# Kernel tuning notes

Hardware: AMD Instinct MI355X
Metric: run time of the kernel (lower is better)

Reference implementation:

```python
import jax, jax.numpy as jnp
import numpy as np

EPS = 1e-12  # F.normalize default eps


def _l2norm(x, axis):
    n = jnp.sqrt(jnp.sum(x * x, axis=axis, keepdims=True))
    return x / jnp.maximum(n, EPS)


def setup_inputs() -> dict:
    key = jax.random.key(0)
    k1, k2, k3, k4 = jax.random.split(key, 4)
    N, T, C, K = 64, 577, 768, 64
    return {
        "grids": jax.random.normal(k1, (N, T, C), dtype=jnp.float32),
        "conv_w": jax.random.normal(k2, (K, C), dtype=jnp.float32) * 0.03,
        "conv_b": jax.random.normal(k3, (K,), dtype=jnp.float32) * 0.01,
        "centroids": jax.random.normal(k4, (K, C), dtype=jnp.float32) * 0.03,
    }


def reference(grids, conv_w, conv_b, centroids):
    # grids: (N, 577, 768) -> (N, C=768, T=577), matching view+permute in torch
    N = grids.shape[0]
    x = jnp.transpose(grids.reshape(N, 577, 768), (0, 2, 1))  # (N, C, T)
    # per-token L2 normalization over channel dim
    x = _l2norm(x, axis=1)
    # 1x1 conv == per-token linear: (N, K, T)
    logits = jnp.einsum('kc,nct->nkt', conv_w, x) + conv_b[None, :, None]
    a = jax.nn.softmax(logits, axis=1)  # softmax over regions K
    # NetVLAD algebraic rewrite of sum_t a[n,k,t]*(x[n,:,t]-c[k,:]):
    #   = (a @ x^T)[n,k,c] - sum_t(a)[n,k] * c[k,c]
    p = jnp.einsum('nkt,nct->nkc', a, x) - a.sum(axis=-1)[:, :, None] * centroids[None]
    p = _l2norm(p, axis=2)             # intra-region normalization
    p = p.reshape(N, -1)               # (N, K*C)
    p = _l2norm(p, axis=1)             # global normalization
    return p
```

## Files before the change

kernel.cpp:

```cpp
#include <hip/hip_runtime.h>
#include <hip/hip_bf16.h>
#include <math.h>

#define TT 577
#define TP 640
#define CCH 768
#define KR 64
#define NB 64
#define LSTR 136

typedef __attribute__((ext_vector_type(8))) short bf16x8;
typedef __attribute__((ext_vector_type(8))) unsigned short ushort8;
typedef __attribute__((ext_vector_type(4))) float f32x4;

static constexpr float EPSF = 1e-12f;

static __device__ inline unsigned short f2bf(float f) {
    return __bfloat16_as_ushort(__float2bfloat16(f));
}
static __device__ inline float bf2f(unsigned short b) {
    union { unsigned int u; float f; } v; v.u = ((unsigned int)b) << 16;
    return v.f;
}

__global__ __launch_bounds__(256) void k_prep(
    const float* __restrict__ conv_w,
    unsigned short* __restrict__ ws_w,
    unsigned short* __restrict__ ws_a)
{
    const int g = blockIdx.x * 256 + threadIdx.x;
    if (g < 6144) {
        const float* s = conv_w + (size_t)g * 8;
        float4 v0 = *reinterpret_cast<const float4*>(s);
        float4 v1 = *reinterpret_cast<const float4*>(s + 4);
        ushort8 o;
        o[0]=f2bf(v0.x); o[1]=f2bf(v0.y); o[2]=f2bf(v0.z); o[3]=f2bf(v0.w);
        o[4]=f2bf(v1.x); o[5]=f2bf(v1.y); o[6]=f2bf(v1.z); o[7]=f2bf(v1.w);
        *reinterpret_cast<ushort8*>(ws_w + (size_t)g * 8) = o;
    }
    if (g < 4096) {
        unsigned short* d = ws_a + (size_t)g * TP + 592;
        ushort8 z = {0,0,0,0,0,0,0,0};
        #pragma unroll
        for (int i = 0; i < 6; ++i)
            *reinterpret_cast<ushort8*>(d + i * 8) = z;
    }
}

__global__ __launch_bounds__(256, 3) void k_logits(
    const float* __restrict__ grids,
    const unsigned short* __restrict__ ws_w,
    const float* __restrict__ conv_b,
    unsigned short* __restrict__ ws_a,
    float* __restrict__ ws_asum)
{
    __shared__ __align__(16) unsigned short Gs[2][64 * LSTR];
    __shared__ __align__(16) unsigned short Ws[64 * LSTR];
    __shared__ float asum_lds[4][64];

    const int tid  = threadIdx.x;
    const int lane = tid & 63;
    const int w    = tid >> 6;
    const int n    = blockIdx.x / 10;
    const int tb   = (blockIdx.x - n * 10) << 6;
    const int t0w  = tb + (w << 4);

    const int lr = lane & 15;
    const int lg = lane >> 4;

    const float* gbase = grids + (size_t)n * TT * CCH;

    float4  ga[8];
    ushort8 wa[4];

    #define GLOAD(c0_)                                                        \
        { _Pragma("unroll")                                                   \
          for (int it = 0; it < 8; ++it) {                                    \
              const int f = (it << 8) + tid;                                  \
              const int t = f >> 5, c4 = f & 31;                              \
              ga[it] = (tb + t < TT)                                          \
                  ? *reinterpret_cast<const float4*>(                         \
                        gbase + (size_t)(tb + t) * CCH + (c0_) + (c4 << 2))   \
                  : make_float4(0.f, 0.f, 0.f, 0.f);                          \
          } }

    #define GWRITE(buf_)                                                      \
        { _Pragma("unroll")                                                   \
          for (int it = 0; it < 8; ++it) {                                    \
              const int f = (it << 8) + tid;                                  \
              const int t = f >> 5, c4 = f & 31;                              \
              unsigned short o4[4] = { f2bf(ga[it].x), f2bf(ga[it].y),        \
                                       f2bf(ga[it].z), f2bf(ga[it].w) };      \
              *reinterpret_cast<uint2*>(&Gs[buf_][t * LSTR + (c4 << 2)]) =    \
                  *reinterpret_cast<const uint2*>(o4);                        \
          } }

    #define WLOADD(c0_)                                                       \
        { _Pragma("unroll")                                                   \
          for (int it = 0; it < 4; ++it) {                                    \
              const int f = (it << 8) + tid;                                  \
              const int kr = f >> 4, c8 = f & 15;                             \
              wa[it] = *reinterpret_cast<const ushort8*>(                     \
                  ws_w + (size_t)kr * CCH + (c0_) + (c8 << 3));               \
          } }

    #define WWRITED()                                                         \
        { _Pragma("unroll")                                                   \
          for (int it = 0; it < 4; ++it) {                                    \
              const int f = (it << 8) + tid;                                  \
              const int kr = f >> 4, c8 = f & 15;                             \
              *reinterpret_cast<ushort8*>(&Ws[kr * LSTR + (c8 << 3)]) = wa[it]; \
          } }

    f32x4 acc[4] = {};
    float ss = 0.f;

    GLOAD(0) WLOADD(0)
    GWRITE(0) WWRITED()
    __syncthreads();

    for (int ch = 0; ch < 6; ++ch) {
        if (ch < 5) { GLOAD((ch + 1) << 7) WLOADD((ch + 1) << 7) }

        const unsigned short* Gb = &Gs[ch & 1][0];
        #pragma unroll
        for (int s = 0; s < 4; ++s) {
            const int cl = (s << 5) + (lg << 3);
            bf16x8 af = *reinterpret_cast<const bf16x8*>(
                &Gb[((w << 4) + lr) * LSTR + cl]);
            #pragma unroll
            for (int j = 0; j < 8; ++j) {
                const float v = bf2f(((unsigned short*)&af)[j]);
                ss = fmaf(v, v, ss);
            }
            bf16x8 b0 = *reinterpret_cast<const bf16x8*>(&Ws[ lr        * LSTR + cl]);
            bf16x8 b1 = *reinterpret_cast<const bf16x8*>(&Ws[(16 + lr) * LSTR + cl]);
            bf16x8 b2 = *reinterpret_cast<const bf16x8*>(&Ws[(32 + lr) * LSTR + cl]);
            bf16x8 b3 = *reinterpret_cast<const bf16x8*>(&Ws[(48 + lr) * LSTR + cl]);
            acc[0] = __builtin_amdgcn_mfma_f32_16x16x32_bf16(af, b0, acc[0], 0, 0, 0);
            acc[1] = __builtin_amdgcn_mfma_f32_16x16x32_bf16(af, b1, acc[1], 0, 0, 0);
            acc[2] = __builtin_amdgcn_mfma_f32_16x16x32_bf16(af, b2, acc[2], 0, 0, 0);
            acc[3] = __builtin_amdgcn_mfma_f32_16x16x32_bf16(af, b3, acc[3], 0, 0, 0);
        }

        if (ch < 5) {
            __syncthreads();
            GWRITE((ch + 1) & 1) WWRITED()
            __syncthreads();
        }
    }

    ss += __shfl_xor(ss, 16);
    ss += __shfl_xor(ss, 32);
    const float nrm = sqrtf(ss);
    const float inv = 1.0f / fmaxf(nrm, EPSF);

    float b_[4];
    #pragma unroll
    for (int rt = 0; rt < 4; ++rt) b_[rt] = conv_b[rt*16 + lr];

    float invT[4];
    #pragma unroll
    for (int reg = 0; reg < 4; ++reg) invT[reg] = __shfl(inv, (lg << 2) + reg);

    float lgt[4][4], mx[4];
    #pragma unroll
    for (int reg = 0; reg < 4; ++reg) {
        float m = -1e30f;
        #pragma unroll
        for (int rt = 0; rt < 4; ++rt) {
            lgt[rt][reg] = fmaf(acc[rt][reg], invT[reg], b_[rt]);
            m = fmaxf(m, lgt[rt][reg]);
        }
        mx[reg] = m;
    }
    #pragma unroll
    for (int msk = 1; msk < 16; msk <<= 1) {
        #pragma unroll
        for (int reg = 0; reg < 4; ++reg) mx[reg] = fmaxf(mx[reg], __shfl_xor(mx[reg], msk));
    }
    float ex[4][4], sm[4] = {0.f, 0.f, 0.f, 0.f};
    #pragma unroll
    for (int rt = 0; rt < 4; ++rt) {
        #pragma unroll
        for (int reg = 0; reg < 4; ++reg) {
            ex[rt][reg] = __expf(lgt[rt][reg] - mx[reg]);
            sm[reg] += ex[rt][reg];
        }
    }
    #pragma unroll
    for (int msk = 1; msk < 16; msk <<= 1) {
        #pragma unroll
        for (int reg = 0; reg < 4; ++reg) sm[reg] += __shfl_xor(sm[reg], msk);
    }

    float rsm[4];
    #pragma unroll
    for (int reg = 0; reg < 4; ++reg) {
        const bool vt = (t0w + (lg << 2) + reg) < TT;
        rsm[reg] = vt ? (1.0f / sm[reg]) : 0.f;
    }

    float pa[4];
    #pragma unroll
    for (int rt = 0; rt < 4; ++rt) {
        pa[rt] = ex[rt][0]*rsm[0] + ex[rt][1]*rsm[1] + ex[rt][2]*rsm[2] + ex[rt][3]*rsm[3];
        pa[rt] += __shfl_xor(pa[rt], 16);
        pa[rt] += __shfl_xor(pa[rt], 32);
    }
    if (lane < 16) {
        #pragma unroll
        for (int rt = 0; rt < 4; ++rt)
            asum_lds[w][rt*16 + lane] = pa[rt];
    }

    unsigned short* Abuf = &Gs[0][0] + (size_t)w * KR * 24;
    #pragma unroll
    for (int reg = 0; reg < 4; ++reg) {
        const int trow = (lg << 2) + reg;
        const float scale = invT[reg] * rsm[reg];
        #pragma unroll
        for (int rt = 0; rt < 4; ++rt)
            Abuf[(rt*16 + lr)*24 + trow] = f2bf(ex[rt][reg] * scale);
    }
    __syncthreads();

    if (tid < 64)
        ws_asum[(size_t)blockIdx.x * 64 + tid] =
            asum_lds[0][tid] + asum_lds[1][tid] + asum_lds[2][tid] + asum_lds[3][tid];

    {
        ushort8 r0 = *reinterpret_cast<const ushort8*>(&Abuf[lane * 24]);
        ushort8 r1 = *reinterpret_cast<const ushort8*>(&Abuf[lane * 24 + 8]);
        unsigned short* dst = ws_a + ((size_t)n * KR + lane) * TP + t0w;
        *reinterpret_cast<ushort8*>(dst)     = r0;
        *reinterpret_cast<ushort8*>(dst + 8) = r1;
    }
}

#define LOADA(d0,d1,d2,d3,t0_)                                                   \
    d0 = *reinterpret_cast<const bf16x8*>(abase +           (size_t)(t0_));      \
    d1 = *reinterpret_cast<const bf16x8*>(abase + 16*TP +   (size_t)(t0_));      \
    d2 = *reinterpret_cast<const bf16x8*>(abase + 32*TP +   (size_t)(t0_));      \
    d3 = *reinterpret_cast<const bf16x8*>(abase + 48*TP +   (size_t)(t0_));

#define LOADB(d,t0_) do {                                                        \
    const int tb2_ = (t0_) + (lg << 3);                                          \
    if ((t0_) + 32 <= TT) {                                                      \
        _Pragma("unroll")                                                        \
        for (int j_ = 0; j_ < 8; ++j_)                                           \
            ((unsigned short*)&(d))[j_] = f2bf(gb[(size_t)(tb2_ + j_) * CCH]);   \
    } else {                                                                     \
        _Pragma("unroll")                                                        \
        for (int j_ = 0; j_ < 8; ++j_) {                                         \
            float v_ = (tb2_ + j_ < TT) ? gb[(size_t)(tb2_ + j_) * CCH] : 0.f;   \
            ((unsigned short*)&(d))[j_] = f2bf(v_);                              \
        }                                                                        \
    } } while (0)

__global__ __launch_bounds__(256, 4) void k_vlad(
    const float* __restrict__ grids,
    const unsigned short* __restrict__ ws_a,
    const float* __restrict__ ws_asum,
    const float* __restrict__ centroids,
    float* __restrict__ out)
{
    __shared__ float asum_s[64];

    const int tid  = threadIdx.x;
    const int lane = tid & 63;
    const int w    = tid >> 6;
    const int n    = blockIdx.x / 12;
    const int c0   = (blockIdx.x - n * 12) << 6;
    const int lr   = lane & 15;
    const int lg   = lane >> 4;

    if (tid < 64) {
        float s = 0.f;
        #pragma unroll
        for (int b = 0; b < 10; ++b)
            s += ws_asum[((size_t)n * 10 + b) * 64 + tid];
        asum_s[tid] = s;
    }
    __syncthreads();

    const int c = c0 + (w << 4) + lr;
    const unsigned short* abase = ws_a + ((size_t)n * KR + lr) * TP + (lg << 3);
    const float* gb = grids + (size_t)n * TT * CCH + c;

    f32x4 acc0 = {}, acc1 = {}, acc2 = {}, acc3 = {};
    bf16x8 a0, a1, a2, a3, b0;
    bf16x8 p0, p1, p2, p3, q0;

    LOADA(a0, a1, a2, a3, 0)
    LOADB(b0, 0);

    int t0 = 0;
    while (true) {
        int tn = t0 + 32;
        if (tn < TT) { LOADA(p0, p1, p2, p3, tn) LOADB(q0, tn); }
        acc0 = __builtin_amdgcn_mfma_f32_16x16x32_bf16(a0, b0, acc0, 0, 0, 0);
        acc1 = __builtin_amdgcn_mfma_f32_16x16x32_bf16(a1, b0, acc1, 0, 0, 0);
        acc2 = __builtin_amdgcn_mfma_f32_16x16x32_bf16(a2, b0, acc2, 0, 0, 0);
        acc3 = __builtin_amdgcn_mfma_f32_16x16x32_bf16(a3, b0, acc3, 0, 0, 0);
        t0 = tn;
        if (t0 >= TT) break;

        tn = t0 + 32;
        if (tn < TT) { LOADA(a0, a1, a2, a3, tn) LOADB(b0, tn); }
        acc0 = __builtin_amdgcn_mfma_f32_16x16x32_bf16(p0, q0, acc0, 0, 0, 0);
        acc1 = __builtin_amdgcn_mfma_f32_16x16x32_bf16(p1, q0, acc1, 0, 0, 0);
        acc2 = __builtin_amdgcn_mfma_f32_16x16x32_bf16(p2, q0, acc2, 0, 0, 0);
        acc3 = __builtin_amdgcn_mfma_f32_16x16x32_bf16(p3, q0, acc3, 0, 0, 0);
        t0 = tn;
        if (t0 >= TT) break;
    }

    #pragma unroll
    for (int reg = 0; reg < 4; ++reg) {
        {
            const int kr = 0*16 + (lg << 2) + reg;
            out[((size_t)n * KR + kr) * CCH + c] =
                acc0[reg] - asum_s[kr] * centroids[(size_t)kr * CCH + c];
        }
        {
            const int kr = 1*16 + (lg << 2) + reg;
            out[((size_t)n * KR + kr) * CCH + c] =
                acc1[reg] - asum_s[kr] * centroids[(size_t)kr * CCH + c];
        }
        {
            const int kr = 2*16 + (lg << 2) + reg;
            out[((size_t)n * KR + kr) * CCH + c] =
                acc2[reg] - asum_s[kr] * centroids[(size_t)kr * CCH + c];
        }
        {
            const int kr = 3*16 + (lg << 2) + reg;
            out[((size_t)n * KR + kr) * CCH + c] =
                acc3[reg] - asum_s[kr] * centroids[(size_t)kr * CCH + c];
        }
    }
}

__global__ __launch_bounds__(256) void kc_norm_kernel(float* __restrict__ out)
{
    const int tid = threadIdx.x;
    const int sub = tid >> 6;
    const int l   = tid & 63;
    float4* p = reinterpret_cast<float4*>(out) + ((size_t)blockIdx.x * 4 + sub) * 192;
    float4 v0 = p[l];
    float4 v1 = p[l + 64];
    float4 v2 = p[l + 128];
    float ss = v0.x*v0.x + v0.y*v0.y + v0.z*v0.z + v0.w*v0.w
             + v1.x*v1.x + v1.y*v1.y + v1.z*v1.z + v1.w*v1.w
             + v2.x*v2.x + v2.y*v2.y + v2.z*v2.z + v2.w*v2.w;
    #pragma unroll
    for (int m = 1; m < 64; m <<= 1) ss += __shfl_xor(ss, m);
    const float sc = 0.125f / fmaxf(sqrtf(ss), EPSF);
    v0.x*=sc; v0.y*=sc; v0.z*=sc; v0.w*=sc;
    v1.x*=sc; v1.y*=sc; v1.z*=sc; v1.w*=sc;
    v2.x*=sc; v2.y*=sc; v2.z*=sc; v2.w*=sc;
    p[l] = v0;
    p[l + 64] = v1;
    p[l + 128] = v2;
}

extern "C" void kernel_launch(void* const* d_in, const int* in_sizes, int n_in,
                              void* d_out, int out_size, void* d_ws, size_t ws_size,
                              hipStream_t stream)
{
    const float* grids     = (const float*)d_in[0];
    const float* conv_w    = (const float*)d_in[1];
    const float* conv_b    = (const float*)d_in[2];
    const float* centroids = (const float*)d_in[3];
    float* out = (float*)d_out;

    unsigned short* ws_a    = (unsigned short*)d_ws;
    float*          ws_asum = (float*)((char*)d_ws + 5242880);
    unsigned short* ws_w    = (unsigned short*)((char*)d_ws + 5406720);

    hipLaunchKernelGGL(k_prep, dim3(24), dim3(256), 0, stream,
                       conv_w, ws_w, ws_a);
    hipLaunchKernelGGL(k_logits, dim3(NB * 10), dim3(256), 0, stream,
                       grids, ws_w, conv_b, ws_a, ws_asum);
    hipLaunchKernelGGL(k_vlad, dim3(NB * 12), dim3(256), 0, stream,
                       grids, ws_a, ws_asum, centroids, out);
    hipLaunchKernelGGL(kc_norm_kernel, dim3(NB * KR / 4), dim3(256), 0, stream, out);
}
```

Measured before the change: 78.83 us.

## Restructure logits kernel into 32-token slabs with split-K waves and XCD swizzle

The logits kernel now loads a whole 32-token by 768-channel slab of grids into LDS as bf16 up front, instead of double-buffering 64-token chunks. Four waves split the work two ways by token half and two ways by channel half, then reduce partial logits and sums of squares through LDS before the softmax. The grid grows from 10 to 19 blocks per batch, so there are more blocks and better load balance. Block indices in both logits and vlad are remapped round-robin across 8 groups, apparently to spread work across XCDs. The cost is more LDS, lower occupancy (launch bounds 2), an extra LDS reduction, and idle waves during the softmax phase.

```diff
diff --git a/kernel.cpp b/kernel.cpp
--- a/kernel.cpp
+++ b/kernel.cpp
@@ -7,7 +7,8 @@
 #define CCH 768
 #define KR 64
 #define NB 64
-#define LSTR 136
+#define SLAB 32
+#define NSLAB 19
 
 typedef __attribute__((ext_vector_type(8))) short bf16x8;
 typedef __attribute__((ext_vector_type(8))) unsigned short ushort8;
@@ -39,200 +40,218 @@
         *reinterpret_cast<ushort8*>(ws_w + (size_t)g * 8) = o;
     }
     if (g < 4096) {
-        unsigned short* d = ws_a + (size_t)g * TP + 592;
+        unsigned short* d = ws_a + (size_t)g * TP + 608;
         ushort8 z = {0,0,0,0,0,0,0,0};
         #pragma unroll
-        for (int i = 0; i < 6; ++i)
+        for (int i = 0; i < 4; ++i)
             *reinterpret_cast<ushort8*>(d + i * 8) = z;
     }
 }
 
-__global__ __launch_bounds__(256, 3) void k_logits(
+__global__ __launch_bounds__(256, 2) void k_logits(
     const float* __restrict__ grids,
     const unsigned short* __restrict__ ws_w,
     const float* __restrict__ conv_b,
     unsigned short* __restrict__ ws_a,
     float* __restrict__ ws_asum)
 {
-    __shared__ __align__(16) unsigned short Gs[2][64 * LSTR];
-    __shared__ __align__(16) unsigned short Ws[64 * LSTR];
-    __shared__ float asum_lds[4][64];
+    __shared__ __align__(16) unsigned short Xs[SLAB * 776];
+    __shared__ __align__(16) unsigned short Wl[KR * 136];
+    __shared__ float ssl[2][2][16];
+    __shared__ float asum_lds[2][64];
 
     const int tid  = threadIdx.x;
     const int lane = tid & 63;
     const int w    = tid >> 6;
-    const int n    = blockIdx.x / 10;
-    const int tb   = (blockIdx.x - n * 10) << 6;
-    const int t0w  = tb + (w << 4);
+    const int p    = w & 1;
+    const int h    = w >> 1;
+    const int b    = (blockIdx.x & 7) * 152 + (blockIdx.x >> 3);
+    const int n    = b / NSLAB;
+    const int sb   = b - n * NSLAB;
+    const int t0   = sb << 5;
 
     const int lr = lane & 15;
     const int lg = lane >> 4;
 
-    const float* gbase = grids + (size_t)n * TT * CCH;
-
-    float4  ga[8];
     ushort8 wa[4];
-
-    #define GLOAD(c0_)                                                        \
-        { _Pragma("unroll")                                                   \
-          for (int it = 0; it < 8; ++it) {                                    \
-              const int f = (it << 8) + tid;                                  \
-              const int t = f >> 5, c4 = f & 31;                              \
-              ga[it] = (tb + t < TT)                                          \
-                  ? *reinterpret_cast<const float4*>(                         \
-                        gbase + (size_t)(tb + t) * CCH + (c0_) + (c4 << 2))   \
-                  : make_float4(0.f, 0.f, 0.f, 0.f);                          \
-          } }
-
-    #define GWRITE(buf_)                                                      \
-        { _Pragma("unroll")                                                   \
-          for (int it = 0; it < 8; ++it) {                                    \
-              const int f = (it << 8) + tid;                                  \
-              const int t = f >> 5, c4 = f & 31;                              \
-              unsigned short o4[4] = { f2bf(ga[it].x), f2bf(ga[it].y),        \
-                                       f2bf(ga[it].z), f2bf(ga[it].w) };      \
-              *reinterpret_cast<uint2*>(&Gs[buf_][t * LSTR + (c4 << 2)]) =    \
-                  *reinterpret_cast<const uint2*>(o4);                        \
-          } }
-
-    #define WLOADD(c0_)                                                       \
-        { _Pragma("unroll")                                                   \
-          for (int it = 0; it < 4; ++it) {                                    \
-              const int f = (it << 8) + tid;                                  \
-              const int kr = f >> 4, c8 = f & 15;                             \
-              wa[it] = *reinterpret_cast<const ushort8*>(                     \
-                  ws_w + (size_t)kr * CCH + (c0_) + (c8 << 3));               \
-          } }
-
-    #define WWRITED()                                                         \
-        { _Pragma("unroll")                                                   \
-          for (int it = 0; it < 4; ++it) {                                    \
-              const int f = (it << 8) + tid;                                  \
-              const int kr = f >> 4, c8 = f & 15;                             \
-              *reinterpret_cast<ushort8*>(&Ws[kr * LSTR + (c8 << 3)]) = wa[it]; \
-          } }
+    auto wload = [&](int ch) {
+        const int c0 = ch << 7;
+        #pragma unroll
+        for (int it = 0; it < 4; ++it) {
+            const int kr = it * 16 + (tid >> 4);
+            wa[it] = *reinterpret_cast<const ushort8*>(
+                ws_w + (size_t)kr * CCH + c0 + ((tid & 15) << 3));
+        }
+    };
+    auto wstore = [&]() {
+        #pragma unroll
+        for (int it = 0; it < 4; ++it) {
+            const int kr = it * 16 + (tid >> 4);
+            *reinterpret_cast<ushort8*>(&Wl[kr * 136 + ((tid & 15) << 3)]) = wa[it];
+        }
+    };
+
+    wload(0);
+    {
+        const int lim = TT - t0;
+        const float* gsl = grids + ((size_t)n * TT + t0) * CCH;
+        #pragma unroll
+        for (int it = 0; it < 24; ++it) {
+            const int f  = (it << 8) + tid;
+            const int t  = f / 192;
+            const int c4 = f - t * 192;
+            float4 v = (t < lim)
+                ? *reinterpret_cast<const float4*>(gsl + (size_t)t * CCH + (c4 << 2))
+                : make_float4(0.f, 0.f, 0.f, 0.f);
+            unsigned short o4[4] = { f2bf(v.x), f2bf(v.y), f2bf(v.z), f2bf(v.w) };
+            *reinterpret_cast<uint2*>(&Xs[t * 776 + (c4 << 2)]) =
+                *reinterpret_cast<const uint2*>(o4);
+        }
+    }
+    wstore();
+    __syncthreads();
 
     f32x4 acc[4] = {};
     float ss = 0.f;
-
-    GLOAD(0) WLOADD(0)
-    GWRITE(0) WWRITED()
-    __syncthreads();
+    const int co = h << 6;
 
     for (int ch = 0; ch < 6; ++ch) {
-        if (ch < 5) { GLOAD((ch + 1) << 7) WLOADD((ch + 1) << 7) }
-
-        const unsigned short* Gb = &Gs[ch & 1][0];
-        #pragma unroll
-        for (int s = 0; s < 4; ++s) {
-            const int cl = (s << 5) + (lg << 3);
+        if (ch < 5) wload(ch + 1);
+        const int cb = ch << 7;
+        #pragma unroll
+        for (int s2 = 0; s2 < 2; ++s2) {
+            const int cs = co + (s2 << 5) + (lg << 3);
             bf16x8 af = *reinterpret_cast<const bf16x8*>(
-                &Gb[((w << 4) + lr) * LSTR + cl]);
+                &Xs[(p * 16 + lr) * 776 + cb + cs]);
             #pragma unroll
             for (int j = 0; j < 8; ++j) {
                 const float v = bf2f(((unsigned short*)&af)[j]);
                 ss = fmaf(v, v, ss);
             }
-            bf16x8 b0 = *reinterpret_cast<const bf16x8*>(&Ws[ lr        * LSTR + cl]);
-            bf16x8 b1 = *reinterpret_cast<const bf16x8*>(&Ws[(16 + lr) * LSTR + cl]);
-            bf16x8 b2 = *reinterpret_cast<const bf16x8*>(&Ws[(32 + lr) * LSTR + cl]);
-            bf16x8 b3 = *reinterpret_cast<const bf16x8*>(&Ws[(48 + lr) * LSTR + cl]);
+            bf16x8 b0 = *reinterpret_cast<const bf16x8*>(&Wl[ lr        * 136 + cs]);
+            bf16x8 b1 = *reinterpret_cast<const bf16x8*>(&Wl[(16 + lr) * 136 + cs]);
+            bf16x8 b2 = *reinterpret_cast<const bf16x8*>(&Wl[(32 + lr) * 136 + cs]);
+            bf16x8 b3 = *reinterpret_cast<const bf16x8*>(&Wl[(48 + lr) * 136 + cs]);
             acc[0] = __builtin_amdgcn_mfma_f32_16x16x32_bf16(af, b0, acc[0], 0, 0, 0);
             acc[1] = __builtin_amdgcn_mfma_f32_16x16x32_bf16(af, b1, acc[1], 0, 0, 0);
             acc[2] = __builtin_amdgcn_mfma_f32_16x16x32_bf16(af, b2, acc[2], 0, 0, 0);
             acc[3] = __builtin_amdgcn_mfma_f32_16x16x32_bf16(af, b3, acc[3], 0, 0, 0);
         }
-
-        if (ch < 5) {
-            __syncthreads();
-            GWRITE((ch + 1) & 1) WWRITED()
-            __syncthreads();
-        }
+        __syncthreads();
+        if (ch < 5) { wstore(); __syncthreads(); }
     }
 
     ss += __shfl_xor(ss, 16);
     ss += __shfl_xor(ss, 32);
-    const float nrm = sqrtf(ss);
-    const float inv = 1.0f / fmaxf(nrm, EPSF);
-
-    float b_[4];
-    #pragma unroll
-    for (int rt = 0; rt < 4; ++rt) b_[rt] = conv_b[rt*16 + lr];
-
-    float invT[4];
-    #pragma unroll
-    for (int reg = 0; reg < 4; ++reg) invT[reg] = __shfl(inv, (lg << 2) + reg);
-
-    float lgt[4][4], mx[4];
-    #pragma unroll
-    for (int reg = 0; reg < 4; ++reg) {
-        float m = -1e30f;
-        #pragma unroll
-        for (int rt = 0; rt < 4; ++rt) {
-            lgt[rt][reg] = fmaf(acc[rt][reg], invT[reg], b_[rt]);
-            m = fmaxf(m, lgt[rt][reg]);
-        }
-        mx[reg] = m;
-    }
-    #pragma unroll
-    for (int msk = 1; msk < 16; msk <<= 1) {
-        #pragma unroll
-        for (int reg = 0; reg < 4; ++reg) mx[reg] = fmaxf(mx[reg], __shfl_xor(mx[reg], msk));
-    }
-    float ex[4][4], sm[4] = {0.f, 0.f, 0.f, 0.f};
+    if (lane < 16) ssl[h][p][lane] = ss;
+
+    float* plog = reinterpret_cast<float*>(&Wl[0]);
     #pragma unroll
     for (int rt = 0; rt < 4; ++rt) {
         #pragma unroll
+        for (int reg = 0; reg < 4; ++reg)
+            plog[(((h * 2 + p) * 16) + (lg * 4 + reg)) * 64 + rt * 16 + lr] =
+                acc[rt][reg];
+    }
+    __syncthreads();
+
+    if (w < 2) {
+        const int p2  = w;
+        const int t0w = t0 + (p2 << 4);
+
+        const float ssf = ssl[0][p2][lr] + ssl[1][p2][lr];
+        const float nrm = sqrtf(ssf);
+        const float inv = 1.0f / fmaxf(nrm, EPSF);
+
+        float b_[4];
+        #pragma unroll
+        for (int rt = 0; rt < 4; ++rt) b_[rt] = conv_b[rt * 16 + lr];
+
+        float invT[4];
+        #pragma unroll
+        for (int reg = 0; reg < 4; ++reg) invT[reg] = __shfl(inv, (lg << 2) + reg);
+
+        const float* pl0 = &plog[(p2 * 16) * 64];
+        const float* pl1 = &plog[((2 + p2) * 16) * 64];
+
+        float lgt[4][4], mx[4];
+        #pragma unroll
         for (int reg = 0; reg < 4; ++reg) {
-            ex[rt][reg] = __expf(lgt[rt][reg] - mx[reg]);
-            sm[reg] += ex[rt][reg];
-        }
-    }
-    #pragma unroll
-    for (int msk = 1; msk < 16; msk <<= 1) {
-        #pragma unroll
-        for (int reg = 0; reg < 4; ++reg) sm[reg] += __shfl_xor(sm[reg], msk);
-    }
-
-    float rsm[4];
-    #pragma unroll
-    for (int reg = 0; reg < 4; ++reg) {
-        const bool vt = (t0w + (lg << 2) + reg) < TT;
-        rsm[reg] = vt ? (1.0f / sm[reg]) : 0.f;
-    }
-
-    float pa[4];
-    #pragma unroll
-    for (int rt = 0; rt < 4; ++rt) {
-        pa[rt] = ex[rt][0]*rsm[0] + ex[rt][1]*rsm[1] + ex[rt][2]*rsm[2] + ex[rt][3]*rsm[3];
-        pa[rt] += __shfl_xor(pa[rt], 16);
-        pa[rt] += __shfl_xor(pa[rt], 32);
-    }
-    if (lane < 16) {
-        #pragma unroll
-        for (int rt = 0; rt < 4; ++rt)
-            asum_lds[w][rt*16 + lane] = pa[rt];
-    }
-
-    unsigned short* Abuf = &Gs[0][0] + (size_t)w * KR * 24;
-    #pragma unroll
-    for (int reg = 0; reg < 4; ++reg) {
-        const int trow = (lg << 2) + reg;
-        const float scale = invT[reg] * rsm[reg];
-        #pragma unroll
-        for (int rt = 0; rt < 4; ++rt)
-            Abuf[(rt*16 + lr)*24 + trow] = f2bf(ex[rt][reg] * scale);
+            const int tok = (lg << 2) + reg;
+            float m = -1e30f;
+            #pragma unroll
+            for (int rt = 0; rt < 4; ++rt) {
+                const int k = rt * 16 + lr;
+                const float raw = pl0[tok * 64 + k] + pl1[tok * 64 + k];
+                lgt[rt][reg] = fmaf(raw, invT[reg], b_[rt]);
+                m = fmaxf(m, lgt[rt][reg]);
+            }
+            mx[reg] = m;
+        }
+        #pragma unroll
+        for (int msk = 1; msk < 16; msk <<= 1) {
+            #pragma unroll
+            for (int reg = 0; reg < 4; ++reg)
+                mx[reg] = fmaxf(mx[reg], __shfl_xor(mx[reg], msk));
+        }
+        float ex[4][4], sm[4] = {0.f, 0.f, 0.f, 0.f};
+        #pragma unroll
+        for (int rt = 0; rt < 4; ++rt) {
+            #pragma unroll
+            for (int reg = 0; reg < 4; ++reg) {
+                ex[rt][reg] = __expf(lgt[rt][reg] - mx[reg]);
+                sm[reg] += ex[rt][reg];
+            }
+        }
+        #pragma unroll
+        for (int msk = 1; msk < 16; msk <<= 1) {
+            #pragma unroll
+            for (int reg = 0; reg < 4; ++reg)
+                sm[reg] += __shfl_xor(sm[reg], msk);
+        }
+
+        float rsm[4];
+        #pragma unroll
+        for (int reg = 0; reg < 4; ++reg) {
+            const bool vt = (t0w + (lg << 2) + reg) < TT;
+            rsm[reg] = vt ? (1.0f / sm[reg]) : 0.f;
+        }
+
+        float pa[4];
+        #pragma unroll
+        for (int rt = 0; rt < 4; ++rt) {
+            pa[rt] = ex[rt][0]*rsm[0] + ex[rt][1]*rsm[1]
+                   + ex[rt][2]*rsm[2] + ex[rt][3]*rsm[3];
+            pa[rt] += __shfl_xor(pa[rt], 16);
+            pa[rt] += __shfl_xor(pa[rt], 32);
+        }
+        if (lane < 16) {
+            #pragma unroll
+            for (int rt = 0; rt < 4; ++rt)
+                asum_lds[p2][rt * 16 + lane] = pa[rt];
+        }
+
+        unsigned short* Ab = &Xs[0] + (size_t)p2 * KR * 24;
+        #pragma unroll
+        for (int reg = 0; reg < 4; ++reg) {
+            const int trow = (lg << 2) + reg;
+            const float scale = invT[reg] * rsm[reg];
+            #pragma unroll
+            for (int rt = 0; rt < 4; ++rt)
+                Ab[(rt * 16 + lr) * 24 + trow] = f2bf(ex[rt][reg] * scale);
+        }
     }
     __syncthreads();
 
     if (tid < 64)
-        ws_asum[(size_t)blockIdx.x * 64 + tid] =
-            asum_lds[0][tid] + asum_lds[1][tid] + asum_lds[2][tid] + asum_lds[3][tid];
-
-    {
-        ushort8 r0 = *reinterpret_cast<const ushort8*>(&Abuf[lane * 24]);
-        ushort8 r1 = *reinterpret_cast<const ushort8*>(&Abuf[lane * 24 + 8]);
-        unsigned short* dst = ws_a + ((size_t)n * KR + lane) * TP + t0w;
+        ws_asum[((size_t)n * NSLAB + sb) * 64 + tid] =
+            asum_lds[0][tid] + asum_lds[1][tid];
+
+    if (w < 2) {
+        const unsigned short* Ab = &Xs[0] + (size_t)w * KR * 24;
+        ushort8 r0 = *reinterpret_cast<const ushort8*>(&Ab[lane * 24]);
+        ushort8 r1 = *reinterpret_cast<const ushort8*>(&Ab[lane * 24 + 8]);
+        unsigned short* dst = ws_a + ((size_t)n * KR + lane) * TP + t0 + (w << 4);
         *reinterpret_cast<ushort8*>(dst)     = r0;
         *reinterpret_cast<ushort8*>(dst + 8) = r1;
     }
@@ -270,16 +289,17 @@
     const int tid  = threadIdx.x;
     const int lane = tid & 63;
     const int w    = tid >> 6;
-    const int n    = blockIdx.x / 12;
-    const int c0   = (blockIdx.x - n * 12) << 6;
+    const int b    = (blockIdx.x & 7) * 96 + (blockIdx.x >> 3);
+    const int n    = b / 12;
+    const int c0   = (b - n * 12) << 6;
     const int lr   = lane & 15;
     const int lg   = lane >> 4;
 
     if (tid < 64) {
         float s = 0.f;
         #pragma unroll
-        for (int b = 0; b < 10; ++b)
-            s += ws_asum[((size_t)n * 10 + b) * 64 + tid];
+        for (int bb = 0; bb < NSLAB; ++bb)
+            s += ws_asum[((size_t)n * NSLAB + bb) * 64 + tid];
         asum_s[tid] = s;
     }
     __syncthreads();
@@ -376,11 +396,11 @@
 
     unsigned short* ws_a    = (unsigned short*)d_ws;
     float*          ws_asum = (float*)((char*)d_ws + 5242880);
-    unsigned short* ws_w    = (unsigned short*)((char*)d_ws + 5406720);
+    unsigned short* ws_w    = (unsigned short*)((char*)d_ws + 5554176);
 
     hipLaunchKernelGGL(k_prep, dim3(24), dim3(256), 0, stream,
                        conv_w, ws_w, ws_a);
-    hipLaunchKernelGGL(k_logits, dim3(NB * 10), dim3(256), 0, stream,
+    hipLaunchKernelGGL(k_logits, dim3(NB * NSLAB), dim3(256), 0, stream,
                        grids, ws_w, conv_b, ws_a, ws_asum);
     hipLaunchKernelGGL(k_vlad, dim3(NB * 12), dim3(256), 0, stream,
                        grids, ws_a, ws_asum, centroids, out);
```

After: 93.18 us. 18.2% more time.
